# Kernel optimization log

Hardware: AMD Instinct MI355X
Metric: run time of the kernel (lower is better)

Reference implementation:

```python
import jax, jax.numpy as jnp
import numpy as np

M = 4096      # dictionary_size
D = 64        # feature dim
YD = 4        # output dim (y_dim)
FF = 0.999    # forgetting_factor
REG = 1e-2    # regularisation
JITTER = 1e-10
LS = 8.0      # RBF lengthscale


def rbf(a, b):
    # squared-distance RBF Gram via the ||a||^2 + ||b||^2 - 2ab^T identity
    a2 = jnp.sum(a * a, -1)[:, None]
    b2 = jnp.sum(b * b, -1)[None, :]
    d2 = jnp.maximum(a2 + b2 - 2.0 * (a @ b.T), 0.0)
    return jnp.exp(-d2 / (2.0 * LS * LS))


def setup_inputs() -> dict:
    key = jax.random.key(0)
    ks = jax.random.split(key, 7)
    return {
        'dictionary': jax.random.normal(ks[0], (M, D), jnp.float32),
        'mu': jax.random.normal(ks[1], (YD, M, 1), jnp.float32),
        'sigma': jax.random.normal(ks[2], (M, M), jnp.float32),
        'Q': jax.random.normal(ks[3], (M, M), jnp.float32),
        'x': jax.random.normal(ks[4], (D,), jnp.float32),
        'y': jax.random.normal(ks[5], (YD,), jnp.float32),
        'noise_num': jax.random.uniform(ks[6], (YD, 1, 1), jnp.float32),
        'noise_den': jnp.ones((1,), jnp.float32),
        'time_index': jnp.arange(M, dtype=jnp.float32),
        't': M,
    }


def reference(dictionary, mu, sigma, Q, x, y, noise_num, noise_den, time_index, t):
    alloc = time_index >= 0.0                      # (M,) bool: allocated slots
    y_ = y[:, None, None]                          # (YD,1,1)

    # --- B2P forgetting ---
    Kdd = rbf(dictionary, dictionary) * (alloc[:, None] * alloc[None, :])
    sig = FF * sigma + (1.0 - FF) * Kdd
    mu_f = jnp.sqrt(FF) * mu

    # --- kernel evals for new sample ---
    K_dx = rbf(dictionary, x[None, :]) * alloc[:, None]   # (M,1)
    K_xx = rbf(x[None, :], x[None, :]) + JITTER           # (1,1)

    q_ = Q @ K_dx                                         # (M,1)
    pu = jnp.maximum(K_xx - K_dx.T @ q_, 0.0)             # projection uncertainty (1,1)
    h_ = sig @ q_                                         # (M,1)
    npv = jnp.maximum(pu + q_.T @ h_, 0.0)                # noiseless predictive var (1,1)
    pred_mean = q_.T @ mu_f                               # (YD,1,1) via batched matmul
    pv = REG + npv

    # --- augmented (M+1) state ---
    p_ = jnp.concatenate((h_, npv), axis=-2)              # (M+1,1)
    mu_a = jnp.concatenate((mu_f, pred_mean), axis=-2) + (y_ - pred_mean) / pv * p_
    sig_a = jnp.block([[sig, h_], [h_.T, npv]]) - (p_ @ p_.T) / pv
    p2 = jnp.concatenate((q_, -jnp.ones((1, 1), q_.dtype)), axis=0)
    Q_a = jnp.pad(Q, ((0, 1), (0, 1))) + (p2 @ p2.T) / pu

    nnum = noise_num + FF * (y_ - pred_mean) ** 2 / pv
    nden = noise_den + FF

    # --- pruning criterion ---
    x_alloc = jnp.concatenate((alloc, jnp.ones((1,), bool)))

    def crit_low(_):
        return jnp.concatenate((jnp.ones((M, 1), Q_a.dtype), jnp.zeros((1, 1), Q_a.dtype)))

    def crit_mse(_):
        dq = jnp.where(~x_alloc, jnp.inf, jnp.diag(Q_a))
        errors = Q_a @ mu_a / dq[:, None]                 # (YD,M+1,1)
        return jnp.abs(errors).sum(-3)                    # (M+1,1)

    criterion = jax.lax.cond(pu.squeeze() < JITTER, crit_low, crit_mse, None)
    prune = jnp.argmin(criterion)
    denom = jnp.where(~x_alloc[prune], jnp.inf, Q_a[prune, prune])

    # swap (prune <-> last) permutation, then drop last row/col
    perm = jnp.arange(M + 1)
    perm = jnp.where(perm == prune, M, jnp.where(perm == M, prune, perm))

    Q_r = Q_a[perm, :]                                    # row swap
    Qs = Q_r[:-1, prune]                                  # column `prune` after row swap
    Q_n = Q_r[:, perm][:M, :M] - jnp.outer(Qs, Qs) / denom

    mu_n = mu_a[:, perm, :][:, :M, :]
    sig_n = sig_a[perm, :][:, perm][:M, :M]

    dict_n = dictionary.at[prune].set(x)
    ti_n = time_index.at[prune].set(jnp.asarray(t, time_index.dtype))
    alloc_n = ti_n >= 0.0
    sig_n = (alloc_n[:, None] * alloc_n[None, :]) * sig_n
    mu_n = jnp.where((ti_n < 0.0)[:, None], 0.0, mu_n)

    return (mu_n, sig_n, Q_n, dict_n, ti_n, nnum, nden)
```

## Files before the change

### kernel.cpp

```cpp
#include <hip/hip_runtime.h>
#include <math.h>

#define Mn 4096
#define Dn 64
#define MUA_STRIDE 4104

#define OFF_A2   0
#define OFF_CRIT 0
#define OFF_K    4096
#define OFF_Q    8192
#define OFF_H    12288
#define OFF_MUA  16384
#define OFF_QS   32800
#define OFF_QSD  36896
#define SC_PU    40992
#define SC_INVPU 40993
#define SC_NPV   40994
#define SC_PV    40995
#define SC_INVPV 40996
#define SC_DENOM 40997
#define SC_PRUNE 40998

#define O_MU   0
#define O_SIG  16384
#define O_Q    16793600
#define O_DICT 33570816
#define O_TI   33832960
#define O_NNUM 33837056
#define O_NDEN 33837060

__device__ __forceinline__ float waveReduceSum(float v) {
#pragma unroll
    for (int o = 32; o > 0; o >>= 1) v += __shfl_down(v, o);
    return v;
}

__global__ void k1_prep(const float* __restrict__ dict, const float* __restrict__ x,
                        const float* __restrict__ ti, float* __restrict__ ws) {
    int row  = blockIdx.x * 4 + (threadIdx.x >> 6);
    int lane = threadIdx.x & 63;
    float d  = dict[row * Dn + lane];
    float xv = x[lane];
    float a2 = waveReduceSum(d * d);
    float x2 = waveReduceSum(xv * xv);
    float dx = waveReduceSum(d * xv);
    if (lane == 0) {
        ws[OFF_A2 + row] = a2;
        float d2 = fmaxf(a2 + x2 - 2.0f * dx, 0.0f);
        float kv = expf(d2 * (-1.0f / 128.0f));
        ws[OFF_K + row] = (ti[row] >= 0.0f) ? kv : 0.0f;
    }
}

__global__ void k2_q(const float* __restrict__ Q, float* __restrict__ ws) {
    __shared__ float red[4];
    const int row = blockIdx.x;
    const int tid = threadIdx.x;
    const float4* Qr = (const float4*)(Q + (size_t)row * Mn);
    const float4* kv = (const float4*)(ws + OFF_K);
    float s = 0.0f;
#pragma unroll
    for (int it = 0; it < 4; ++it) {
        int u = tid + it * 256;
        float4 a = Qr[u], b = kv[u];
        s += a.x * b.x + a.y * b.y + a.z * b.z + a.w * b.w;
    }
    s = waveReduceSum(s);
    if ((tid & 63) == 0) red[tid >> 6] = s;
    __syncthreads();
    if (tid == 0) {
        ws[OFF_Q + row] = red[0] + red[1] + red[2] + red[3];
        ws[OFF_H + row] = 0.0f;
    }
}

__global__ __launch_bounds__(256, 4) void k3_sig_h(
        const float* __restrict__ dict, const float* __restrict__ sigma,
        const float* __restrict__ ti, float* __restrict__ ws, float* __restrict__ out) {
    __shared__ __align__(16) float At[64 * 68];
    __shared__ __align__(16) float Bt[64 * 68];
    __shared__ float hred[64 * 16];
    const int tid = threadIdx.x;
    const int tx = tid & 15, ty = tid >> 4;
    const int r0 = blockIdx.y * 64;
    const int cchunk = blockIdx.x * 128;
    const int pidx = ((tid & 15) << 4) | (tid >> 4);
    const int prow = pidx >> 4;
    const int pcol = (pidx & 15) << 2;

#pragma unroll
    for (int l = 0; l < 4; ++l) {
        int u = pidx + l * 256;
        int row = u >> 4;
        int col = (u & 15) << 2;
        float4 v = *(const float4*)(dict + (size_t)(r0 + row) * Dn + col);
        At[(col + 0) * 68 + row] = v.x;
        At[(col + 1) * 68 + row] = v.y;
        At[(col + 2) * 68 + row] = v.z;
        At[(col + 3) * 68 + row] = v.w;
    }

    float a2i[4], ali[4];
#pragma unroll
    for (int r = 0; r < 4; ++r) {
        int gi = r0 + ty * 4 + r;
        a2i[r] = ws[OFF_A2 + gi];
        ali[r] = (ti[gi] >= 0.0f) ? 1.0f : 0.0f;
    }

    float hacc[4] = {0.f, 0.f, 0.f, 0.f};

    float4 pre[4];
#pragma unroll
    for (int l = 0; l < 4; ++l) {
        int row = (pidx + l * 256) >> 4;
        int col = ((pidx + l * 256) & 15) << 2;
        pre[l] = *(const float4*)(dict + (size_t)(cchunk + row) * Dn + col);
    }

    for (int ct = 0; ct < 2; ++ct) {
        const int c0 = cchunk + ct * 64;
        __syncthreads();
#pragma unroll
        for (int l = 0; l < 4; ++l) {
            int u = pidx + l * 256;
            int row = u >> 4;
            int col = (u & 15) << 2;
            Bt[(col + 0) * 68 + row] = pre[l].x;
            Bt[(col + 1) * 68 + row] = pre[l].y;
            Bt[(col + 2) * 68 + row] = pre[l].z;
            Bt[(col + 3) * 68 + row] = pre[l].w;
        }
        if (ct < 1) {
            const int c1 = cchunk + (ct + 1) * 64;
#pragma unroll
            for (int l = 0; l < 4; ++l) {
                int row = (pidx + l * 256) >> 4;
                int col = ((pidx + l * 256) & 15) << 2;
                pre[l] = *(const float4*)(dict + (size_t)(c1 + row) * Dn + col);
            }
        }
        __syncthreads();

        float acc[4][4];
#pragma unroll
        for (int r = 0; r < 4; ++r)
#pragma unroll
            for (int c = 0; c < 4; ++c) acc[r][c] = 0.0f;

#pragma unroll
        for (int kk = 0; kk < 64; ++kk) {
            float4 av = *(const float4*)(At + kk * 68 + (ty << 2));
            float4 bv = *(const float4*)(Bt + kk * 68 + (tx << 2));
            acc[0][0] = fmaf(av.x, bv.x, acc[0][0]);
            acc[0][1] = fmaf(av.x, bv.y, acc[0][1]);
            acc[0][2] = fmaf(av.x, bv.z, acc[0][2]);
            acc[0][3] = fmaf(av.x, bv.w, acc[0][3]);
            acc[1][0] = fmaf(av.y, bv.x, acc[1][0]);
            acc[1][1] = fmaf(av.y, bv.y, acc[1][1]);
            acc[1][2] = fmaf(av.y, bv.z, acc[1][2]);
            acc[1][3] = fmaf(av.y, bv.w, acc[1][3]);
            acc[2][0] = fmaf(av.z, bv.x, acc[2][0]);
            acc[2][1] = fmaf(av.z, bv.y, acc[2][1]);
            acc[2][2] = fmaf(av.z, bv.z, acc[2][2]);
            acc[2][3] = fmaf(av.z, bv.w, acc[2][3]);
            acc[3][0] = fmaf(av.w, bv.x, acc[3][0]);
            acc[3][1] = fmaf(av.w, bv.y, acc[3][1]);
            acc[3][2] = fmaf(av.w, bv.z, acc[3][2]);
            acc[3][3] = fmaf(av.w, bv.w, acc[3][3]);
        }

        const int j = c0 + tx * 4;
        const float4 a2j4 = *(const float4*)(ws + OFF_A2 + j);
        const float4 qj4  = *(const float4*)(ws + OFF_Q + j);
        const float4 tj4  = *(const float4*)(ti + j);
        float a2j[4] = {a2j4.x, a2j4.y, a2j4.z, a2j4.w};
        float qj[4]  = {qj4.x, qj4.y, qj4.z, qj4.w};
        float alj[4] = {tj4.x >= 0.f ? 1.f : 0.f, tj4.y >= 0.f ? 1.f : 0.f,
                        tj4.z >= 0.f ? 1.f : 0.f, tj4.w >= 0.f ? 1.f : 0.f};

#pragma unroll
        for (int r = 0; r < 4; ++r) {
            const int gi = r0 + ty * 4 + r;
            const size_t off = (size_t)gi * Mn + j;
            const float4 sg = *(const float4*)(sigma + off);
            float sv[4] = {sg.x, sg.y, sg.z, sg.w};
            float res[4];
#pragma unroll
            for (int c = 0; c < 4; ++c) {
                float d2 = fmaxf(a2i[r] + a2j[c] - 2.0f * acc[r][c], 0.0f);
                float kv = __expf(d2 * (-1.0f / 128.0f)) * ali[r] * alj[c];
                res[c] = 0.999f * sv[c] + 0.001f * kv;
                hacc[r] += res[c] * qj[c];
            }
            float4 o = {res[0], res[1], res[2], res[3]};
            *(float4*)(out + O_SIG + off) = o;
        }
    }

    __syncthreads();
#pragma unroll
    for (int r = 0; r < 4; ++r) hred[(ty * 4 + r) * 16 + tx] = hacc[r];
    __syncthreads();
    if (tid < 64) {
        float s = 0.0f;
#pragma unroll
        for (int c = 0; c < 16; ++c) s += hred[tid * 16 + c];
        atomicAdd(ws + OFF_H + r0 + tid, s);
    }
}

__device__ __forceinline__ float blockReduce1024(float v, float* sred) {
    v = waveReduceSum(v);
    int tid = threadIdx.x;
    __syncthreads();
    if ((tid & 63) == 0) sred[tid >> 6] = v;
    __syncthreads();
    float r = 0.0f;
    if (tid == 0) {
#pragma unroll
        for (int i = 0; i < 16; ++i) r += sred[i];
    }
    return r;
}

__global__ __launch_bounds__(1024) void k4_scalars(
        const float* __restrict__ mu, const float* __restrict__ y,
        const float* __restrict__ nn, const float* __restrict__ nd,
        float* __restrict__ ws, float* __restrict__ out) {
    __shared__ float sred[16];
    __shared__ float sb[8];
    const int tid = threadIdx.x;
    const float* k = ws + OFF_K;
    const float* q = ws + OFF_Q;
    const float* h = ws + OFF_H;
    float kq = 0, qh = 0, p0 = 0, p1 = 0, p2 = 0, p3 = 0;
    for (int i = tid; i < Mn; i += 1024) {
        float qi = q[i];
        kq += k[i] * qi;
        qh += qi * h[i];
        p0 += qi * mu[0 * Mn + i];
        p1 += qi * mu[1 * Mn + i];
        p2 += qi * mu[2 * Mn + i];
        p3 += qi * mu[3 * Mn + i];
    }
    float rkq = blockReduce1024(kq, sred);
    float rqh = blockReduce1024(qh, sred);
    float r0 = blockReduce1024(p0, sred);
    float r1 = blockReduce1024(p1, sred);
    float r2 = blockReduce1024(p2, sred);
    float r3 = blockReduce1024(p3, sred);
    if (tid == 0) {
        const float sf = sqrtf(0.999f);
        float pu  = fmaxf(1.0f - rkq, 0.0f);
        float npv = fmaxf(pu + rqh, 0.0f);
        float pv  = 0.01f + npv;
        ws[SC_PU] = pu;
        ws[SC_INVPU] = 1.0f / pu;
        ws[SC_NPV] = npv;
        ws[SC_PV] = pv;
        ws[SC_INVPV] = 1.0f / pv;
        float pm[4] = {sf * r0, sf * r1, sf * r2, sf * r3};
#pragma unroll
        for (int yd = 0; yd < 4; ++yd) {
            float yv = y[yd];
            float dy = yv - pm[yd];
            float dl = dy / pv;
            sb[yd] = dl;
            ws[OFF_MUA + yd * MUA_STRIDE + Mn] = pm[yd] + dl * npv;
            out[O_NNUM + yd] = nn[yd] + 0.999f * (dy * dy) / pv;
        }
        out[O_NDEN] = nd[0] + 0.999f;
    }
    __syncthreads();
    const float sf = sqrtf(0.999f);
    float d0 = sb[0], d1 = sb[1], d2 = sb[2], d3 = sb[3];
    for (int i = tid; i < Mn; i += 1024) {
        float hi = h[i];
        ws[OFF_MUA + 0 * MUA_STRIDE + i] = sf * mu[0 * Mn + i] + d0 * hi;
        ws[OFF_MUA + 1 * MUA_STRIDE + i] = sf * mu[1 * Mn + i] + d1 * hi;
        ws[OFF_MUA + 2 * MUA_STRIDE + i] = sf * mu[2 * Mn + i] + d2 * hi;
        ws[OFF_MUA + 3 * MUA_STRIDE + i] = sf * mu[3 * Mn + i] + d3 * hi;
    }
}

__global__ __launch_bounds__(256) void k5_crit(const float* __restrict__ Q,
                                               const float* __restrict__ ti,
                                               float* __restrict__ ws) {
    __shared__ float sred[4][4];
    const int row = blockIdx.x;
    const int tid = threadIdx.x;
    const float pu = ws[SC_PU];
    if (pu < 1e-10f) {
        if (tid == 0) ws[OFF_CRIT + row] = (row < Mn) ? 1.0f : 0.0f;
        return;
    }
    const float inv_pu = ws[SC_INVPU];
    const bool rin = (row < Mn);
    const float p2i = rin ? ws[OFF_Q + row] : -1.0f;
    const float4* q4  = (const float4*)(ws + OFF_Q);
    const float4* Qr4 = (const float4*)(Q + (size_t)row * Mn);
    const float* mua = ws + OFF_MUA;
    float n0 = 0, n1 = 0, n2 = 0, n3 = 0;
#pragma unroll
    for (int it = 0; it < 4; ++it) {
        int u = tid + it * 256;
        float4 qv = q4[u];
        float4 base = rin ? Qr4[u] : make_float4(0.f, 0.f, 0.f, 0.f);
        float4 qa;
        qa.x = base.x + p2i * qv.x * inv_pu;
        qa.y = base.y + p2i * qv.y * inv_pu;
        qa.z = base.z + p2i * qv.z * inv_pu;
        qa.w = base.w + p2i * qv.w * inv_pu;
        const float4 m0 = *(const float4*)(mua + 0 * MUA_STRIDE + u * 4);
        const float4 m1 = *(const float4*)(mua + 1 * MUA_STRIDE + u * 4);
        const float4 m2 = *(const float4*)(mua + 2 * MUA_STRIDE + u * 4);
        const float4 m3 = *(const float4*)(mua + 3 * MUA_STRIDE + u * 4);
        n0 += qa.x * m0.x + qa.y * m0.y + qa.z * m0.z + qa.w * m0.w;
        n1 += qa.x * m1.x + qa.y * m1.y + qa.z * m1.z + qa.w * m1.w;
        n2 += qa.x * m2.x + qa.y * m2.y + qa.z * m2.z + qa.w * m2.w;
        n3 += qa.x * m3.x + qa.y * m3.y + qa.z * m3.z + qa.w * m3.w;
    }
    n0 = waveReduceSum(n0);
    n1 = waveReduceSum(n1);
    n2 = waveReduceSum(n2);
    n3 = waveReduceSum(n3);
    if ((tid & 63) == 0) {
        int w = tid >> 6;
        sred[w][0] = n0; sred[w][1] = n1; sred[w][2] = n2; sred[w][3] = n3;
    }
    __syncthreads();
    if (tid == 0) {
        float t0 = 0, t1 = 0, t2 = 0, t3 = 0;
#pragma unroll
        for (int w = 0; w < 4; ++w) {
            t0 += sred[w][0]; t1 += sred[w][1]; t2 += sred[w][2]; t3 += sred[w][3];
        }
        float qaM = -p2i * inv_pu;
        t0 += qaM * mua[0 * MUA_STRIDE + Mn];
        t1 += qaM * mua[1 * MUA_STRIDE + Mn];
        t2 += qaM * mua[2 * MUA_STRIDE + Mn];
        t3 += qaM * mua[3 * MUA_STRIDE + Mn];
        bool xa = rin ? (ti[row] >= 0.0f) : true;
        float crit = 0.0f;
        if (xa) {
            float dq = rin ? (Q[(size_t)row * Mn + row] + p2i * p2i * inv_pu) : inv_pu;
            crit = fabsf(t0 / dq) + fabsf(t1 / dq) + fabsf(t2 / dq) + fabsf(t3 / dq);
        }
        ws[OFF_CRIT + row] = crit;
    }
}

__global__ __launch_bounds__(1024) void k6_argmin(const float* __restrict__ Q,
                                                  const float* __restrict__ ti,
                                                  float* __restrict__ ws) {
    __shared__ float sval[1024];
    __shared__ int   sidx[1024];
    const int tid = threadIdx.x;
    float bv = INFINITY;
    int bi = Mn + 1;
    for (int i = tid; i <= Mn; i += 1024) {
        float v = ws[OFF_CRIT + i];
        if (v < bv) { bv = v; bi = i; }
    }
    sval[tid] = bv; sidx[tid] = bi;
    __syncthreads();
    for (int s = 512; s > 0; s >>= 1) {
        if (tid < s) {
            float ov = sval[tid + s]; int oi = sidx[tid + s];
            if (ov < sval[tid] || (ov == sval[tid] && oi < sidx[tid])) {
                sval[tid] = ov; sidx[tid] = oi;
            }
        }
        __syncthreads();
    }
    if (tid == 0) {
        int prune = sidx[0];
        ((int*)ws)[SC_PRUNE] = prune;
        float inv_pu = ws[SC_INVPU];
        bool xa = (prune == Mn) ? true : (ti[prune] >= 0.0f);
        float qap;
        if (prune < Mn) {
            float qp = ws[OFF_Q + prune];
            qap = Q[(size_t)prune * Mn + prune] + qp * qp * inv_pu;
        } else {
            qap = inv_pu;
        }
        ws[SC_DENOM] = xa ? qap : INFINITY;
    }
}

__global__ void k6b_vec(const float* __restrict__ Q, const float* __restrict__ dict,
                        const float* __restrict__ x, const float* __restrict__ ti,
                        const int* __restrict__ tptr, float* __restrict__ ws,
                        float* __restrict__ out) {
    const int tid = blockIdx.x * 256 + threadIdx.x;
    const int prune = ((const int*)ws)[SC_PRUNE];
    const int row = tid >> 6, col = tid & 63;
    out[O_DICT + tid] = (row == prune) ? x[col] : dict[tid];
    if (tid < Mn) {
        float tv = ti[tid];
        if (tid == prune) {
            int raw = *tptr;
            tv = (raw >= 0 && raw < (1 << 30)) ? (float)raw : __int_as_float(raw);
        }
        out[O_TI + tid] = tv;
        const float inv_pu = ws[SC_INVPU];
        const float denom  = ws[SC_DENOM];
        const float p2p = (prune < Mn) ? ws[OFF_Q + prune] : -1.0f;
        float qs;
        if (tid == prune) {
            qs = -p2p * inv_pu;
        } else {
            float base = (prune < Mn) ? Q[(size_t)tid * Mn + prune] : 0.0f;
            qs = base + ws[OFF_Q + tid] * p2p * inv_pu;
        }
        ws[OFF_QS + tid] = qs;
        ws[OFF_QSD + tid] = qs / denom;
    }
}

__global__ __launch_bounds__(256) void k7_fused(const float* __restrict__ Q,
                                                float* __restrict__ out,
                                                const float* __restrict__ ws) {
    const int i = blockIdx.x;
    const int tid = threadIdx.x;
    const int prune = ((const int*)ws)[SC_PRUNE];
    const float inv_pu = ws[SC_INVPU];
    const float inv_pv = ws[SC_INVPV];
    const float npv = ws[SC_NPV];

    const int pi = (i == prune) ? Mn : i;
    const bool piok = (pi < Mn);
    const float p2i = piok ? ws[OFF_Q + pi] : -1.0f;
    const float qsi = ws[OFF_QS + i];
    const float4* Qr4  = (const float4*)(Q + (size_t)pi * Mn);
    const float4* q4   = (const float4*)(ws + OFF_Q);
    const float4* qsd4 = (const float4*)(ws + OFF_QSD);
    float4* o4 = (float4*)(out + O_Q + (size_t)i * Mn);
#pragma unroll
    for (int it = 0; it < 4; ++it) {
        int u = tid + it * 256;
        float4 base = piok ? Qr4[u] : make_float4(0.f, 0.f, 0.f, 0.f);
        float4 p2j = q4[u];
        if ((prune >> 2) == u) {
            int c = prune & 3;
            ((float*)&p2j)[c] = -1.0f;
            ((float*)&base)[c] = 0.0f;
        }
        float4 d = qsd4[u];
        float4 r;
        r.x = base.x + p2i * p2j.x * inv_pu - qsi * d.x;
        r.y = base.y + p2i * p2j.y * inv_pu - qsi * d.y;
        r.z = base.z + p2i * p2j.z * inv_pu - qsi * d.z;
        r.w = base.w + p2i * p2j.w * inv_pu - qsi * d.w;
        o4[u] = r;
    }

    const bool ip = (i == prune);
    const float ai = (out[O_TI + i] >= 0.0f) ? 1.0f : 0.0f;
    const float hi = ws[OFF_H + i];
    const float p_i = ip ? npv : hi;
    const float4* h4  = (const float4*)(ws + OFF_H);
    const float4* ti4 = (const float4*)(out + O_TI);
    float4* s4 = (float4*)(out + O_SIG + (size_t)i * Mn);
#pragma unroll
    for (int it = 0; it < 4; ++it) {
        int u = tid + it * 256;
        float4 sv = s4[u];
        float4 hj = h4[u];
        float4 tv = ti4[u];
        float pj[4] = {hj.x, hj.y, hj.z, hj.w};
        float bs[4];
        if (ip) { bs[0] = hj.x; bs[1] = hj.y; bs[2] = hj.z; bs[3] = hj.w; }
        else    { bs[0] = sv.x; bs[1] = sv.y; bs[2] = sv.z; bs[3] = sv.w; }
        if ((prune >> 2) == u) {
            int c = prune & 3;
            pj[c] = npv;
            bs[c] = ip ? npv : hi;
        }
        float aj[4] = {tv.x >= 0.f ? 1.f : 0.f, tv.y >= 0.f ? 1.f : 0.f,
                       tv.z >= 0.f ? 1.f : 0.f, tv.w >= 0.f ? 1.f : 0.f};
        float4 r;
        r.x = ai * aj[0] * (bs[0] - p_i * pj[0] * inv_pv);
        r.y = ai * aj[1] * (bs[1] - p_i * pj[1] * inv_pv);
        r.z = ai * aj[2] * (bs[2] - p_i * pj[2] * inv_pv);
        r.w = ai * aj[3] * (bs[3] - p_i * pj[3] * inv_pv);
        s4[u] = r;
    }

    if (tid < 4) {
        float tin = out[O_TI + i];
        float v;
        if (tin < 0.0f) v = 0.0f;
        else v = ws[OFF_MUA + tid * MUA_STRIDE + (ip ? Mn : i)];
        out[O_MU + tid * Mn + i] = v;
    }
}

extern "C" void kernel_launch(void* const* d_in, const int* in_sizes, int n_in,
                              void* d_out, int out_size, void* d_ws, size_t ws_size,
                              hipStream_t stream) {
    const float* dict  = (const float*)d_in[0];
    const float* mu    = (const float*)d_in[1];
    const float* sigma = (const float*)d_in[2];
    const float* Q     = (const float*)d_in[3];
    const float* x     = (const float*)d_in[4];
    const float* y     = (const float*)d_in[5];
    const float* nn    = (const float*)d_in[6];
    const float* nd    = (const float*)d_in[7];
    const float* ti    = (const float*)d_in[8];
    const int*   tptr  = (const int*)d_in[9];
    float* out = (float*)d_out;
    float* ws  = (float*)d_ws;

    k1_prep<<<1024, 256, 0, stream>>>(dict, x, ti, ws);
    k2_q<<<4096, 256, 0, stream>>>(Q, ws);
    k3_sig_h<<<dim3(32, 64), 256, 0, stream>>>(dict, sigma, ti, ws, out);
    k4_scalars<<<1, 1024, 0, stream>>>(mu, y, nn, nd, ws, out);
    k5_crit<<<4097, 256, 0, stream>>>(Q, ti, ws);
    k6_argmin<<<1, 1024, 0, stream>>>(Q, ti, ws);
    k6b_vec<<<1024, 256, 0, stream>>>(Q, dict, x, ti, tptr, ws, out);
    k7_fused<<<4096, 256, 0, stream>>>(Q, out, ws);
}
```

Measured before the change: 343.7 us.

## Compute dictionary Gram tile with bf16 MFMA instead of FP32 shared-memory FMA

The dictionary is converted to bf16 in the prep kernel, and the sigma-forgetting kernel now computes the pairwise dot products with 16x16x32 bf16 MFMA instructions directly from registers, without shared-memory staging. This is meant to remove the FP32 FMA inner loop and the LDS traffic of the Gram computation. In exchange, the RBF kernel values lose precision through bf16 dot products, and the sigma read/write becomes scalar per-lane accesses instead of float4 vectors.

```diff
diff --git a/kernel.cpp b/kernel.cpp
--- a/kernel.cpp
+++ b/kernel.cpp
@@ -20,6 +20,7 @@
 #define SC_INVPV 40996
 #define SC_DENOM 40997
 #define SC_PRUNE 40998
+#define OFF_DICTB 49152
 
 #define O_MU   0
 #define O_SIG  16384
@@ -29,10 +30,19 @@
 #define O_NNUM 33837056
 #define O_NDEN 33837060
 
+typedef __attribute__((ext_vector_type(8))) __bf16 bf16x8;
+typedef __attribute__((ext_vector_type(4))) float f32x4;
+
 __device__ __forceinline__ float waveReduceSum(float v) {
 #pragma unroll
     for (int o = 32; o > 0; o >>= 1) v += __shfl_down(v, o);
     return v;
+}
+
+__device__ __forceinline__ unsigned short f2bf_rne(float f) {
+    unsigned u = __float_as_uint(f);
+    unsigned r = (u + 0x7FFFu + ((u >> 16) & 1u)) >> 16;
+    return (unsigned short)r;
 }
 
 __global__ void k1_prep(const float* __restrict__ dict, const float* __restrict__ x,
@@ -41,6 +51,7 @@
     int lane = threadIdx.x & 63;
     float d  = dict[row * Dn + lane];
     float xv = x[lane];
+    ((unsigned short*)(ws + OFF_DICTB))[row * Dn + lane] = f2bf_rne(d);
     float a2 = waveReduceSum(d * d);
     float x2 = waveReduceSum(xv * xv);
     float dx = waveReduceSum(d * xv);
@@ -74,140 +85,82 @@
     }
 }
 
-__global__ __launch_bounds__(256, 4) void k3_sig_h(
-        const float* __restrict__ dict, const float* __restrict__ sigma,
-        const float* __restrict__ ti, float* __restrict__ ws, float* __restrict__ out) {
-    __shared__ __align__(16) float At[64 * 68];
-    __shared__ __align__(16) float Bt[64 * 68];
-    __shared__ float hred[64 * 16];
-    const int tid = threadIdx.x;
-    const int tx = tid & 15, ty = tid >> 4;
-    const int r0 = blockIdx.y * 64;
-    const int cchunk = blockIdx.x * 128;
-    const int pidx = ((tid & 15) << 4) | (tid >> 4);
-    const int prow = pidx >> 4;
-    const int pcol = (pidx & 15) << 2;
-
-#pragma unroll
-    for (int l = 0; l < 4; ++l) {
-        int u = pidx + l * 256;
-        int row = u >> 4;
-        int col = (u & 15) << 2;
-        float4 v = *(const float4*)(dict + (size_t)(r0 + row) * Dn + col);
-        At[(col + 0) * 68 + row] = v.x;
-        At[(col + 1) * 68 + row] = v.y;
-        At[(col + 2) * 68 + row] = v.z;
-        At[(col + 3) * 68 + row] = v.w;
-    }
-
-    float a2i[4], ali[4];
-#pragma unroll
-    for (int r = 0; r < 4; ++r) {
-        int gi = r0 + ty * 4 + r;
-        a2i[r] = ws[OFF_A2 + gi];
-        ali[r] = (ti[gi] >= 0.0f) ? 1.0f : 0.0f;
-    }
-
-    float hacc[4] = {0.f, 0.f, 0.f, 0.f};
-
-    float4 pre[4];
-#pragma unroll
-    for (int l = 0; l < 4; ++l) {
-        int row = (pidx + l * 256) >> 4;
-        int col = ((pidx + l * 256) & 15) << 2;
-        pre[l] = *(const float4*)(dict + (size_t)(cchunk + row) * Dn + col);
-    }
-
-    for (int ct = 0; ct < 2; ++ct) {
-        const int c0 = cchunk + ct * 64;
-        __syncthreads();
-#pragma unroll
-        for (int l = 0; l < 4; ++l) {
-            int u = pidx + l * 256;
-            int row = u >> 4;
-            int col = (u & 15) << 2;
-            Bt[(col + 0) * 68 + row] = pre[l].x;
-            Bt[(col + 1) * 68 + row] = pre[l].y;
-            Bt[(col + 2) * 68 + row] = pre[l].z;
-            Bt[(col + 3) * 68 + row] = pre[l].w;
-        }
-        if (ct < 1) {
-            const int c1 = cchunk + (ct + 1) * 64;
-#pragma unroll
-            for (int l = 0; l < 4; ++l) {
-                int row = (pidx + l * 256) >> 4;
-                int col = ((pidx + l * 256) & 15) << 2;
-                pre[l] = *(const float4*)(dict + (size_t)(c1 + row) * Dn + col);
+__global__ __launch_bounds__(256) void k3_mfma(
+        const float* __restrict__ sigma, const float* __restrict__ ti,
+        float* __restrict__ ws, float* __restrict__ out) {
+    const int tid  = threadIdx.x;
+    const int lane = tid & 63;
+    const int w    = tid >> 6;
+    const int i0 = blockIdx.y * 128 + (w >> 1) * 64;
+    const int j0 = blockIdx.x * 128 + (w & 1) * 64;
+    const int lr = lane >> 4;
+    const int lc = lane & 15;
+
+    const uint4* db = (const uint4*)(ws + OFF_DICTB);
+
+    bf16x8 bfrag[4][2];
+    float a2j[4], qj[4], alj[4];
+#pragma unroll
+    for (int jt = 0; jt < 4; ++jt) {
+        const int col = j0 + jt * 16 + lc;
+        bfrag[jt][0] = __builtin_bit_cast(bf16x8, db[col * 8 + lr]);
+        bfrag[jt][1] = __builtin_bit_cast(bf16x8, db[col * 8 + 4 + lr]);
+        a2j[jt] = ws[OFF_A2 + col];
+        qj[jt]  = ws[OFF_Q + col];
+        alj[jt] = (ti[col] >= 0.0f) ? 1.0f : 0.0f;
+    }
+
+    float hacc[4][4];
+#pragma unroll
+    for (int it = 0; it < 4; ++it)
+#pragma unroll
+        for (int i = 0; i < 4; ++i) hacc[it][i] = 0.0f;
+
+#pragma unroll
+    for (int it = 0; it < 4; ++it) {
+        const int arow = i0 + it * 16 + lc;
+        bf16x8 af0 = __builtin_bit_cast(bf16x8, db[arow * 8 + lr]);
+        bf16x8 af1 = __builtin_bit_cast(bf16x8, db[arow * 8 + 4 + lr]);
+        float a2i[4], ali[4];
+#pragma unroll
+        for (int i = 0; i < 4; ++i) {
+            const int rg = i0 + it * 16 + lr * 4 + i;
+            a2i[i] = ws[OFF_A2 + rg];
+            ali[i] = (ti[rg] >= 0.0f) ? 1.0f : 0.0f;
+        }
+#pragma unroll
+        for (int jt = 0; jt < 4; ++jt) {
+            f32x4 acc = {0.0f, 0.0f, 0.0f, 0.0f};
+            acc = __builtin_amdgcn_mfma_f32_16x16x32_bf16(af0, bfrag[jt][0], acc, 0, 0, 0);
+            acc = __builtin_amdgcn_mfma_f32_16x16x32_bf16(af1, bfrag[jt][1], acc, 0, 0, 0);
+            const int colg = j0 + jt * 16 + lc;
+#pragma unroll
+            for (int i = 0; i < 4; ++i) {
+                const int rg = i0 + it * 16 + lr * 4 + i;
+                const size_t off = (size_t)rg * Mn + colg;
+                float sv  = sigma[off];
+                float d2  = fmaxf(a2i[i] + a2j[jt] - 2.0f * acc[i], 0.0f);
+                float kv  = __expf(d2 * (-1.0f / 128.0f)) * ali[i] * alj[jt];
+                float res = 0.999f * sv + 0.001f * kv;
+                out[O_SIG + off] = res;
+                hacc[it][i] += res * qj[jt];
             }
         }
-        __syncthreads();
-
-        float acc[4][4];
-#pragma unroll
-        for (int r = 0; r < 4; ++r)
-#pragma unroll
-            for (int c = 0; c < 4; ++c) acc[r][c] = 0.0f;
-
-#pragma unroll
-        for (int kk = 0; kk < 64; ++kk) {
-            float4 av = *(const float4*)(At + kk * 68 + (ty << 2));
-            float4 bv = *(const float4*)(Bt + kk * 68 + (tx << 2));
-            acc[0][0] = fmaf(av.x, bv.x, acc[0][0]);
-            acc[0][1] = fmaf(av.x, bv.y, acc[0][1]);
-            acc[0][2] = fmaf(av.x, bv.z, acc[0][2]);
-            acc[0][3] = fmaf(av.x, bv.w, acc[0][3]);
-            acc[1][0] = fmaf(av.y, bv.x, acc[1][0]);
-            acc[1][1] = fmaf(av.y, bv.y, acc[1][1]);
-            acc[1][2] = fmaf(av.y, bv.z, acc[1][2]);
-            acc[1][3] = fmaf(av.y, bv.w, acc[1][3]);
-            acc[2][0] = fmaf(av.z, bv.x, acc[2][0]);
-            acc[2][1] = fmaf(av.z, bv.y, acc[2][1]);
-            acc[2][2] = fmaf(av.z, bv.z, acc[2][2]);
-            acc[2][3] = fmaf(av.z, bv.w, acc[2][3]);
-            acc[3][0] = fmaf(av.w, bv.x, acc[3][0]);
-            acc[3][1] = fmaf(av.w, bv.y, acc[3][1]);
-            acc[3][2] = fmaf(av.w, bv.z, acc[3][2]);
-            acc[3][3] = fmaf(av.w, bv.w, acc[3][3]);
-        }
-
-        const int j = c0 + tx * 4;
-        const float4 a2j4 = *(const float4*)(ws + OFF_A2 + j);
-        const float4 qj4  = *(const float4*)(ws + OFF_Q + j);
-        const float4 tj4  = *(const float4*)(ti + j);
-        float a2j[4] = {a2j4.x, a2j4.y, a2j4.z, a2j4.w};
-        float qj[4]  = {qj4.x, qj4.y, qj4.z, qj4.w};
-        float alj[4] = {tj4.x >= 0.f ? 1.f : 0.f, tj4.y >= 0.f ? 1.f : 0.f,
-                        tj4.z >= 0.f ? 1.f : 0.f, tj4.w >= 0.f ? 1.f : 0.f};
-
-#pragma unroll
-        for (int r = 0; r < 4; ++r) {
-            const int gi = r0 + ty * 4 + r;
-            const size_t off = (size_t)gi * Mn + j;
-            const float4 sg = *(const float4*)(sigma + off);
-            float sv[4] = {sg.x, sg.y, sg.z, sg.w};
-            float res[4];
-#pragma unroll
-            for (int c = 0; c < 4; ++c) {
-                float d2 = fmaxf(a2i[r] + a2j[c] - 2.0f * acc[r][c], 0.0f);
-                float kv = __expf(d2 * (-1.0f / 128.0f)) * ali[r] * alj[c];
-                res[c] = 0.999f * sv[c] + 0.001f * kv;
-                hacc[r] += res[c] * qj[c];
+    }
+
+#pragma unroll
+    for (int it = 0; it < 4; ++it)
+#pragma unroll
+        for (int i = 0; i < 4; ++i) {
+            float v = hacc[it][i];
+            v += __shfl_xor(v, 1);
+            v += __shfl_xor(v, 2);
+            v += __shfl_xor(v, 4);
+            v += __shfl_xor(v, 8);
+            if (lc == (it * 4 + i)) {
+                atomicAdd(ws + OFF_H + i0 + it * 16 + lr * 4 + i, v);
             }
-            float4 o = {res[0], res[1], res[2], res[3]};
-            *(float4*)(out + O_SIG + off) = o;
-        }
-    }
-
-    __syncthreads();
-#pragma unroll
-    for (int r = 0; r < 4; ++r) hred[(ty * 4 + r) * 16 + tx] = hacc[r];
-    __syncthreads();
-    if (tid < 64) {
-        float s = 0.0f;
-#pragma unroll
-        for (int c = 0; c < 16; ++c) s += hred[tid * 16 + c];
-        atomicAdd(ws + OFF_H + r0 + tid, s);
-    }
+        }
 }
 
 __device__ __forceinline__ float blockReduce1024(float v, float* sred) {
@@ -516,7 +469,7 @@
 
     k1_prep<<<1024, 256, 0, stream>>>(dict, x, ti, ws);
     k2_q<<<4096, 256, 0, stream>>>(Q, ws);
-    k3_sig_h<<<dim3(32, 64), 256, 0, stream>>>(dict, sigma, ti, ws, out);
+    k3_mfma<<<dim3(32, 32), 256, 0, stream>>>(sigma, ti, ws, out);
     k4_scalars<<<1, 1024, 0, stream>>>(mu, y, nn, nd, ws, out);
     k5_crit<<<4097, 256, 0, stream>>>(Q, ti, ws);
     k6_argmin<<<1, 1024, 0, stream>>>(Q, ti, ws);
```

New measurement: 340.2 us. Within noise of the previous version (-1.0%).
